# Optimization experiments

Measured on AMD Instinct MI355X. Metric: run time of the kernel, lower is better.

The kernel has to match this reference:

```python
import jax, jax.numpy as jnp
import numpy as np

THRESHOLD = 0.045
TAU = 20.0
N = 1048576
H = 128


def setup_inputs() -> dict:
    key = jax.random.key(0)
    ks = jax.random.split(key, 7)
    x = jax.random.normal(ks[0], (N, 1), dtype=jnp.float32)
    s1 = 1.0  # 1/sqrt(fan_in=1)
    s2 = 1.0 / np.sqrt(H).astype(np.float32)
    W1 = jax.random.uniform(ks[1], (H, 1), jnp.float32, -s1, s1)
    b1 = jax.random.uniform(ks[2], (H,), jnp.float32, -s1, s1)
    W2 = jax.random.uniform(ks[3], (H, H), jnp.float32, -s2, s2)
    b2 = jax.random.uniform(ks[4], (H,), jnp.float32, -s2, s2)
    W3 = jax.random.uniform(ks[5], (1, H), jnp.float32, -s2, s2)
    b3 = jax.random.uniform(ks[6], (1,), jnp.float32, -s2, s2)
    return {"x": x, "W1": W1, "b1": b1, "W2": W2, "b2": b2, "W3": W3, "b3": b3}


def reference(x, W1, b1, W2, b2, W3, b3):
    n = x.shape[0]
    # threshold-gated event mask (mask[0] forced active, as in original)
    diff = jnp.abs(x - jnp.roll(x, 1, axis=0))[:, 0]
    mask = (diff > THRESHOLD).at[0].set(True)
    # tiny MLP; computed densely — values at non-active rows are never read
    # (output gathers only last-active rows), so the math matches the
    # original's gather-then-MLP exactly.
    h = jax.nn.relu(x @ W1.T + b1)        # [N, H]
    h = jax.nn.relu(h @ W2.T + b2)        # [N, H]
    y = h @ W3.T + b3                     # [N, 1]
    t = jnp.arange(n, dtype=jnp.float32)
    # last active time <= i  (cumsum(mask)-1 indexing into active rows is
    # equivalent to gathering at the last active position)
    last_t = jax.lax.cummax(jnp.where(mask, t, jnp.float32(0.0)))  # [N]
    last_idx = last_t.astype(jnp.int32)
    decay = jnp.exp(-(t - last_t) / TAU)[:, None]  # [N, 1]
    output = y[last_idx] * decay
    n_active = mask.sum(dtype=jnp.int32)
    return output, n_active
```

## Files before the change

### kernel.cpp

```cpp
#include <hip/hip_runtime.h>
#include <math.h>


#define THRESH   0.045f
#define NH       128
#define TSZ      8192
#define GMIN     -6.0f
#define GMAX     6.0f
#define TPB      256
#define ITEMS    16
#define CHUNK    (TPB * ITEMS)
#define NSCAN    256
#define POISON32 0xAAAAAAAAu

__global__ __launch_bounds__(TPB) void kT(const float* __restrict__ W1,
                                          const float* __restrict__ b1,
                                          const float* __restrict__ W2,
                                          const float* __restrict__ b2,
                                          const float* __restrict__ W3,
                                          const float* __restrict__ b3,
                                          float* __restrict__ table) {
  __shared__ float w2s[NH * NH];
  const int t = threadIdx.x, b = blockIdx.x;
  {
    const float4* src = (const float4*)W2;
    float4* dst = (float4*)w2s;
    #pragma unroll
    for (int i = 0; i < (NH * NH / 4) / TPB; ++i)
      dst[t + i * TPB] = src[t + i * TPB];
  }
  __syncthreads();

  const int p  = t & 7;
  const int e0 = b * 64 + (t >> 3) * 2;
  const float step = (GMAX - GMIN) * (1.0f / (float)(TSZ - 1));
  const float xv0 = GMIN + step * (float)e0;
  const float xv1 = xv0 + step;

  float h10[16], h11[16];
  #pragma unroll
  for (int c = 0; c < 4; ++c) {
    #pragma unroll
    for (int r = 0; r < 4; ++r) {
      const int k = 4 * (p + 8 * c) + r;
      const float w = W1[k], bb = b1[k];
      h10[c * 4 + r] = fmaxf(fmaf(xv0, w, bb), 0.0f);
      h11[c * 4 + r] = fmaxf(fmaf(xv1, w, bb), 0.0f);
    }
  }
  const bool hi = (p & 4) != 0;
  float y = 0.0f;
  const float b3v = b3[0];
  #pragma unroll 4
  for (int j = 0; j < NH; ++j) {
    const float* row = &w2s[j * NH];
    float a0 = 0.f, a1 = 0.f, c0 = 0.f, c1 = 0.f;
    #pragma unroll
    for (int c = 0; c < 4; ++c) {
      const float4 w = *(const float4*)&row[4 * (p + 8 * c)];
      a0 = fmaf(h10[c * 4 + 0], w.x, a0);
      a1 = fmaf(h10[c * 4 + 1], w.y, a1);
      a0 = fmaf(h10[c * 4 + 2], w.z, a0);
      a1 = fmaf(h10[c * 4 + 3], w.w, a1);
      c0 = fmaf(h11[c * 4 + 0], w.x, c0);
      c1 = fmaf(h11[c * 4 + 1], w.y, c1);
      c0 = fmaf(h11[c * 4 + 2], w.z, c0);
      c1 = fmaf(h11[c * 4 + 3], w.w, c1);
    }
    const float s0 = a0 + a1, s1 = c0 + c1;
    float u = hi ? s1 : s0;
    float v = hi ? s0 : s1;
    v = __shfl_xor(v, 4);
    u += v;
    u += __shfl_xor(u, 1);
    u += __shfl_xor(u, 2);
    const float h2 = fmaxf(u + b2[j], 0.0f);
    y = fmaf(h2, W3[j], y);
  }
  if ((p & 3) == 0) table[e0 + (p >> 2)] = y + b3v;
}

__global__ __launch_bounds__(TPB) void kS(const float* __restrict__ x, int n,
                                          int nblk,
                                          const float* __restrict__ table,
                                          unsigned int* __restrict__ cnts,
                                          float* __restrict__ out) {
  __shared__ int swl[4], swc[4], sred[4];
  __shared__ int sgx;
  const int t = threadIdx.x, b = blockIdx.x;
  const int lane = t & 63, wv = t >> 6;
  const int base = b * CHUNK + t * ITEMS;

  float xs[ITEMS];
  const bool full = (base + ITEMS) <= n;
  if (full) {
    const float4* xv = (const float4*)(x + base);
    #pragma unroll
    for (int q = 0; q < 4; ++q) {
      const float4 v = xv[q];
      xs[q * 4 + 0] = v.x; xs[q * 4 + 1] = v.y;
      xs[q * 4 + 2] = v.z; xs[q * 4 + 3] = v.w;
    }
  } else {
    #pragma unroll
    for (int it = 0; it < ITEMS; ++it)
      xs[it] = (base + it < n) ? x[base + it] : 0.0f;
  }
  float prev = (base > 0 && base <= n) ? x[base - 1] : 0.0f;
  unsigned m = 0; int tl = -1; int cnt = 0;
  #pragma unroll
  for (int it = 0; it < ITEMS; ++it) {
    const int i = base + it;
    if (i < n) {
      const bool act = (i == 0) || (fabsf(xs[it] - prev) > THRESH);
      if (act) { tl = i; ++cnt; m |= (1u << it); }
      prev = xs[it];
    }
  }

  int incl = tl;
  #pragma unroll
  for (int off = 1; off < 64; off <<= 1) {
    const int v = __shfl_up(incl, off);
    if (lane >= off) incl = max(incl, v);
  }
  int wsum = cnt;
  #pragma unroll
  for (int off = 1; off < 64; off <<= 1) wsum += __shfl_xor(wsum, off);
  if (lane == 63) swl[wv] = incl;
  if (lane == 0)  swc[wv] = wsum;

  if (wv == 0) {
    int g = -1;
    if (b > 0) {
      int ws = b * CHUNK - 64;
      for (;;) {
        const int i = ws + lane;
        const float xi = x[i];
        const float xp = (i > 0) ? x[i - 1] : 0.0f;
        const bool act = (i == 0) || (fabsf(xi - xp) > THRESH);
        const unsigned long long bal = __ballot(act);
        if (bal) { g = ws + 63 - (int)__builtin_clzll(bal); break; }
        ws -= 64;
      }
    }
    if (lane == 0) sgx = g;
  }
  __syncthreads();

  const int exclW = __shfl_up(incl, 1);
  int run = sgx;
  #pragma unroll
  for (int w = 0; w < 4; ++w) if (w < wv) run = max(run, swl[w]);
  if (lane > 0) run = max(run, exclW);

  if (t == 0) {
    const int bcnt = swc[0] + swc[1] + swc[2] + swc[3];
    __hip_atomic_store(&cnts[b], (unsigned)(bcnt + 1),
                       __ATOMIC_RELAXED, __HIP_MEMORY_SCOPE_AGENT);
  }

  const float invstep = (float)(TSZ - 1) / (GMAX - GMIN);
  if (full) {
    #pragma unroll
    for (int q = 0; q < 4; ++q) {
      float o[4];
      #pragma unroll
      for (int r = 0; r < 4; ++r) {
        const int it = q * 4 + r;
        const int i = base + it;
        const bool act = (m >> it) & 1u;
        if (act) run = i;
        const float xj = act ? xs[it] : x[run];
        const float u = (xj - GMIN) * invstep;
        int i0 = (int)u;
        i0 = max(0, min(i0, TSZ - 2));
        const float f = u - (float)i0;
        const float t0 = table[i0], t1 = table[i0 + 1];
        const float yv = fmaf(f, t1 - t0, t0);
        o[r] = yv * __expf((float)(run - i) * 0.05f);
      }
      float4 ov = { o[0], o[1], o[2], o[3] };
      ((float4*)(out + base))[q] = ov;
    }
  } else {
    #pragma unroll
    for (int it = 0; it < ITEMS; ++it) {
      const int i = base + it;
      if (i >= n) break;
      const bool act = (m >> it) & 1u;
      if (act) run = i;
      const float xj = act ? xs[it] : x[run];
      const float u = (xj - GMIN) * invstep;
      int i0 = (int)u;
      i0 = max(0, min(i0, TSZ - 2));
      const float f = u - (float)i0;
      const float t0 = table[i0], t1 = table[i0 + 1];
      out[i] = fmaf(f, t1 - t0, t0) * __expf((float)(run - i) * 0.05f);
    }
  }

  if (b == 0) {
    int v = 0;
    if (t < nblk) {
      unsigned c;
      for (;;) {
        c = __hip_atomic_load(&cnts[t], __ATOMIC_RELAXED,
                              __HIP_MEMORY_SCOPE_AGENT);
        if (c != POISON32) break;
        __builtin_amdgcn_s_sleep(1);
      }
      v = (int)c - 1;
    }
    #pragma unroll
    for (int off = 1; off < 64; off <<= 1) v += __shfl_xor(v, off);
    if (lane == 0) sred[wv] = v;
    __syncthreads();
    if (t == 0) out[n] = (float)(sred[0] + sred[1] + sred[2] + sred[3]);
  }
}

extern "C" void kernel_launch(void* const* d_in, const int* in_sizes, int n_in,
                              void* d_out, int out_size, void* d_ws, size_t ws_size,
                              hipStream_t stream) {
  const float* x  = (const float*)d_in[0];
  const float* W1 = (const float*)d_in[1];
  const float* b1 = (const float*)d_in[2];
  const float* W2 = (const float*)d_in[3];
  const float* b2 = (const float*)d_in[4];
  const float* W3 = (const float*)d_in[5];
  const float* b3 = (const float*)d_in[6];
  float* out = (float*)d_out;
  const int n = in_sizes[0];

  char* w = (char*)d_ws;
  float* table = (float*)w;
  unsigned int* cnts = (unsigned int*)(w + TSZ * 4);

  kT<<<TSZ / 64, TPB, 0, stream>>>(W1, b1, W2, b2, W3, b3, table);
  kS<<<NSCAN, TPB, 0, stream>>>(x, n, NSCAN, table, cnts, out);
}
```

Measured before the change: 94.01 us.

## Split table build and scan work across more, smaller blocks

```diff
diff --git a/kernel.cpp b/kernel.cpp
--- a/kernel.cpp
+++ b/kernel.cpp
@@ -8,9 +8,10 @@
 #define GMIN     -6.0f
 #define GMAX     6.0f
 #define TPB      256
-#define ITEMS    16
+#define ITEMS    2
 #define CHUNK    (TPB * ITEMS)
-#define NSCAN    256
+#define NSCAN    2048
+#define NTBLK    256
 #define POISON32 0xAAAAAAAAu
 
 __global__ __launch_bounds__(TPB) void kT(const float* __restrict__ W1,
@@ -31,24 +32,24 @@
   }
   __syncthreads();
 
-  const int p  = t & 7;
-  const int e0 = b * 64 + (t >> 3) * 2;
+  const int p  = t & 15;
+  const int e0 = b * 32 + (t >> 4) * 2;
   const float step = (GMAX - GMIN) * (1.0f / (float)(TSZ - 1));
   const float xv0 = GMIN + step * (float)e0;
   const float xv1 = xv0 + step;
 
-  float h10[16], h11[16];
-  #pragma unroll
-  for (int c = 0; c < 4; ++c) {
+  float h10[8], h11[8];
+  #pragma unroll
+  for (int c = 0; c < 2; ++c) {
     #pragma unroll
     for (int r = 0; r < 4; ++r) {
-      const int k = 4 * (p + 8 * c) + r;
+      const int k = 4 * (p + 16 * c) + r;
       const float w = W1[k], bb = b1[k];
       h10[c * 4 + r] = fmaxf(fmaf(xv0, w, bb), 0.0f);
       h11[c * 4 + r] = fmaxf(fmaf(xv1, w, bb), 0.0f);
     }
   }
-  const bool hi = (p & 4) != 0;
+  const bool hi = (p & 8) != 0;
   float y = 0.0f;
   const float b3v = b3[0];
   #pragma unroll 4
@@ -56,8 +57,8 @@
     const float* row = &w2s[j * NH];
     float a0 = 0.f, a1 = 0.f, c0 = 0.f, c1 = 0.f;
     #pragma unroll
-    for (int c = 0; c < 4; ++c) {
-      const float4 w = *(const float4*)&row[4 * (p + 8 * c)];
+    for (int c = 0; c < 2; ++c) {
+      const float4 w = *(const float4*)&row[4 * (p + 16 * c)];
       a0 = fmaf(h10[c * 4 + 0], w.x, a0);
       a1 = fmaf(h10[c * 4 + 1], w.y, a1);
       a0 = fmaf(h10[c * 4 + 2], w.z, a0);
@@ -70,18 +71,18 @@
     const float s0 = a0 + a1, s1 = c0 + c1;
     float u = hi ? s1 : s0;
     float v = hi ? s0 : s1;
-    v = __shfl_xor(v, 4);
+    v = __shfl_xor(v, 8);
     u += v;
     u += __shfl_xor(u, 1);
     u += __shfl_xor(u, 2);
+    u += __shfl_xor(u, 4);
     const float h2 = fmaxf(u + b2[j], 0.0f);
     y = fmaf(h2, W3[j], y);
   }
-  if ((p & 3) == 0) table[e0 + (p >> 2)] = y + b3v;
+  if ((p & 7) == 0) table[e0 + (p >> 3)] = y + b3v;
 }
 
 __global__ __launch_bounds__(TPB) void kS(const float* __restrict__ x, int n,
-                                          int nblk,
                                           const float* __restrict__ table,
                                           unsigned int* __restrict__ cnts,
                                           float* __restrict__ out) {
@@ -94,13 +95,8 @@
   float xs[ITEMS];
   const bool full = (base + ITEMS) <= n;
   if (full) {
-    const float4* xv = (const float4*)(x + base);
-    #pragma unroll
-    for (int q = 0; q < 4; ++q) {
-      const float4 v = xv[q];
-      xs[q * 4 + 0] = v.x; xs[q * 4 + 1] = v.y;
-      xs[q * 4 + 2] = v.z; xs[q * 4 + 3] = v.w;
-    }
+    const float2 v = *(const float2*)(x + base);
+    xs[0] = v.x; xs[1] = v.y;
   } else {
     #pragma unroll
     for (int it = 0; it < ITEMS; ++it)
@@ -162,27 +158,22 @@
 
   const float invstep = (float)(TSZ - 1) / (GMAX - GMIN);
   if (full) {
-    #pragma unroll
-    for (int q = 0; q < 4; ++q) {
-      float o[4];
-      #pragma unroll
-      for (int r = 0; r < 4; ++r) {
-        const int it = q * 4 + r;
-        const int i = base + it;
-        const bool act = (m >> it) & 1u;
-        if (act) run = i;
-        const float xj = act ? xs[it] : x[run];
-        const float u = (xj - GMIN) * invstep;
-        int i0 = (int)u;
-        i0 = max(0, min(i0, TSZ - 2));
-        const float f = u - (float)i0;
-        const float t0 = table[i0], t1 = table[i0 + 1];
-        const float yv = fmaf(f, t1 - t0, t0);
-        o[r] = yv * __expf((float)(run - i) * 0.05f);
-      }
-      float4 ov = { o[0], o[1], o[2], o[3] };
-      ((float4*)(out + base))[q] = ov;
-    }
+    float o[ITEMS];
+    #pragma unroll
+    for (int it = 0; it < ITEMS; ++it) {
+      const int i = base + it;
+      const bool act = (m >> it) & 1u;
+      if (act) run = i;
+      const float xj = act ? xs[it] : x[run];
+      const float u = (xj - GMIN) * invstep;
+      int i0 = (int)u;
+      i0 = max(0, min(i0, TSZ - 2));
+      const float f = u - (float)i0;
+      const float t0 = table[i0], t1 = table[i0 + 1];
+      o[it] = fmaf(f, t1 - t0, t0) * __expf((float)(run - i) * 0.05f);
+    }
+    float2 ov = { o[0], o[1] };
+    *(float2*)(out + base) = ov;
   } else {
     #pragma unroll
     for (int it = 0; it < ITEMS; ++it) {
@@ -202,15 +193,17 @@
 
   if (b == 0) {
     int v = 0;
-    if (t < nblk) {
+    #pragma unroll
+    for (int s8 = 0; s8 < NSCAN / TPB; ++s8) {
+      const int idx = t + s8 * TPB;
       unsigned c;
       for (;;) {
-        c = __hip_atomic_load(&cnts[t], __ATOMIC_RELAXED,
+        c = __hip_atomic_load(&cnts[idx], __ATOMIC_RELAXED,
                               __HIP_MEMORY_SCOPE_AGENT);
         if (c != POISON32) break;
         __builtin_amdgcn_s_sleep(1);
       }
-      v = (int)c - 1;
+      v += (int)c - 1;
     }
     #pragma unroll
     for (int off = 1; off < 64; off <<= 1) v += __shfl_xor(v, off);
@@ -237,6 +230,6 @@
   float* table = (float*)w;
   unsigned int* cnts = (unsigned int*)(w + TSZ * 4);
 
-  kT<<<TSZ / 64, TPB, 0, stream>>>(W1, b1, W2, b2, W3, b3, table);
-  kS<<<NSCAN, TPB, 0, stream>>>(x, n, NSCAN, table, cnts, out);
+  kT<<<NTBLK, TPB, 0, stream>>>(W1, b1, W2, b2, W3, b3, table);
+  kS<<<NSCAN, TPB, 0, stream>>>(x, n, table, cnts, out);
 }
```

New measurement: 90.89 us (median of 2 runs). 3.3% less time.
